# Kernel tuning notes

Measured on AMD Instinct MI355X. Metric: run time of the kernel, lower is better.

## Reference

```python
import jax, jax.numpy as jnp
import numpy as np

LEAKY_SLOPE = 0.01  # torch nn.LeakyReLU default


def leaky_relu(x):
    return jnp.where(x >= 0, x, LEAKY_SLOPE * x)


def rgcn_conv(x, edge_index, edge_type, w_rel, w_root, b_conv):
    # PyG RGCNConv: out = x @ W_root + b + sum_r mean_{edges of rel r into i}(x_src @ W_r)
    n = x.shape[0]
    src, dst = edge_index[0], edge_index[1]
    out = x @ w_root + b_conv
    num_rel = w_rel.shape[0]
    for r in range(num_rel):  # small fixed relation count
        mask = (edge_type == r)
        msg = x[src] @ w_rel[r]                      # [E, H]
        msg = jnp.where(mask[:, None], msg, 0.0)
        agg = jax.ops.segment_sum(msg, dst, num_segments=n)          # [N, H]
        cnt = jax.ops.segment_sum(mask.astype(x.dtype), dst, num_segments=n)
        out = out + agg / jnp.maximum(cnt, 1.0)[:, None]             # mean aggr
    return out


def setup_inputs() -> dict:
    key = jax.random.key(0)
    ks = jax.random.split(key, 10)
    N, E, D_IN, H, OUT, R = 50000, 600000, 768, 128, 3, 2
    s_in = 1.0 / np.sqrt(D_IN)
    s_h = 1.0 / np.sqrt(H)
    return {
        "feature": jax.random.normal(ks[0], (N, D_IN), dtype=jnp.float32),
        "edge_index": jax.random.randint(ks[1], (2, E), 0, N, dtype=jnp.int64),
        "edge_type": jax.random.randint(ks[2], (E,), 0, R, dtype=jnp.int64),
        "w_in": jax.random.uniform(ks[3], (D_IN, H), jnp.float32, -s_in, s_in),
        "b_in": jax.random.uniform(ks[4], (H,), jnp.float32, -s_in, s_in),
        "w_rel": jax.random.uniform(ks[5], (R, H, H), jnp.float32, -s_h, s_h),
        "w_root": jax.random.uniform(ks[6], (H, H), jnp.float32, -s_h, s_h),
        "b_conv": jnp.zeros((H,), jnp.float32),
        "w_out": jax.random.uniform(ks[7], (H, OUT), jnp.float32, -s_h, s_h),
        "b_out": jax.random.uniform(ks[8], (OUT,), jnp.float32, -s_h, s_h),
    }


def reference(feature, edge_index, edge_type, w_in, b_in, w_rel, w_root, b_conv, w_out, b_out):
    x = leaky_relu(feature @ w_in + b_in)
    # NOTE: original forward applies rgcn1 twice (shared weights); dropout is
    # identity at inference; rgcn2/linear_relu_output1 are unused.
    x = rgcn_conv(x, edge_index, edge_type, w_rel, w_root, b_conv)
    x = rgcn_conv(x, edge_index, edge_type, w_rel, w_root, b_conv)
    return x @ w_out + b_out
```

## Files before the change

### kernel.cpp

```cpp
#include <hip/hip_runtime.h>

#define H 128
#define CAP 64

typedef _Float16 f16x8 __attribute__((ext_vector_type(8)));
typedef float    f32x4 __attribute__((ext_vector_type(4)));

__global__ __launch_bounds__(256) void hist_fill(const int* __restrict__ src,
    const int* __restrict__ dst, const int* __restrict__ et,
    int* __restrict__ cnt, int* __restrict__ elist, int E, int N)
{
    int e = blockIdx.x * 256 + threadIdx.x;
    if (e >= E) return;
    int s = src[e], d = dst[e], t = et[e];
    int b = t * N + d;
    int pos = atomicAdd(&cnt[b], 1);
    if (pos < CAP) elist[(size_t)b * CAP + pos] = s;
}

__global__ __launch_bounds__(256) void prep_w(const float* __restrict__ w_in,
    const float* __restrict__ w_root, const float* __restrict__ w_rel,
    _Float16* __restrict__ wInT, _Float16* __restrict__ w3T, int K)
{
    int idx = blockIdx.x * 256 + threadIdx.x;
    int tot1 = K * H;
    if (idx < tot1) {
        int c = idx / K, k = idx - c * K;
        wInT[idx] = (_Float16)w_in[(size_t)k * H + c];
    } else {
        int i2 = idx - tot1;
        if (i2 < 3 * H * H) {
            int m = i2 / (H * H), r2 = i2 - m * (H * H);
            int c = r2 >> 7, k = r2 & 127;
            const float* s = (m == 0) ? w_root : (w_rel + (size_t)(m - 1) * H * H);
            w3T[i2] = (_Float16)s[(size_t)k * H + c];
        }
    }
}

__device__ __forceinline__ f16x8 cvt8(float4 v0, float4 v1) {
    f16x8 t;
    t[0] = (_Float16)v0.x; t[1] = (_Float16)v0.y; t[2] = (_Float16)v0.z; t[3] = (_Float16)v0.w;
    t[4] = (_Float16)v1.x; t[5] = (_Float16)v1.y; t[6] = (_Float16)v1.z; t[7] = (_Float16)v1.w;
    return t;
}

__global__ __launch_bounds__(256, 4) void gemm_big(const float* __restrict__ A,
    const _Float16* __restrict__ WT, const float* __restrict__ bias,
    _Float16* __restrict__ C16, int M, int K)
{
    __shared__ _Float16 As[2][64][40];
    __shared__ _Float16 Bs[2][128][40];

    const int tid = threadIdx.x;
    const int bm  = blockIdx.x * 64;
    const int w   = tid >> 6;
    const int l   = tid & 63;
    const int l15 = l & 15;
    const int q   = l >> 4;
    const int wr  = (w & 1) * 32;
    const int wc  = (w >> 1) * 64;

    const int sar = tid >> 2;
    const int sak = (tid & 3) * 8;
    int sarow = bm + sar; if (sarow >= M) sarow = M - 1;
    const float* ap = A + (size_t)sarow * K + sak;
    const int sbc = tid >> 1;
    const int sbk = (tid & 1) * 16;
    const _Float16* wp = WT + (size_t)sbc * K + sbk;

    f32x4 acc[2][4];
    const f32x4 z4 = {0.f, 0.f, 0.f, 0.f};
#pragma unroll
    for (int i = 0; i < 2; i++)
#pragma unroll
        for (int j = 0; j < 4; j++) acc[i][j] = z4;

    {
        float4 a0 = *(const float4*)(ap);
        float4 a1 = *(const float4*)(ap + 4);
        f16x8 b0  = *(const f16x8*)(wp);
        f16x8 b1  = *(const f16x8*)(wp + 8);
        *(f16x8*)&As[0][sar][sak]     = cvt8(a0, a1);
        *(f16x8*)&Bs[0][sbc][sbk]     = b0;
        *(f16x8*)&Bs[0][sbc][sbk + 8] = b1;
    }
    __syncthreads();

    const int steps = K / 32;
#pragma unroll 2
    for (int s = 0; s < steps; s++) {
        const int cur = s & 1;
        const bool more = (s + 1) < steps;
        float4 na0, na1; f16x8 nb0, nb1;
        if (more) {
            const int k0 = (s + 1) * 32;
            na0 = *(const float4*)(ap + k0);
            na1 = *(const float4*)(ap + k0 + 4);
            nb0 = *(const f16x8*)(wp + k0);
            nb1 = *(const f16x8*)(wp + k0 + 8);
        }
        f16x8 af[2], bf[4];
#pragma unroll
        for (int i = 0; i < 2; i++) af[i] = *(const f16x8*)&As[cur][wr + i * 16 + l15][q * 8];
#pragma unroll
        for (int j = 0; j < 4; j++) bf[j] = *(const f16x8*)&Bs[cur][wc + j * 16 + l15][q * 8];
#pragma unroll
        for (int i = 0; i < 2; i++)
#pragma unroll
            for (int j = 0; j < 4; j++)
                acc[i][j] = __builtin_amdgcn_mfma_f32_16x16x32_f16(af[i], bf[j], acc[i][j], 0, 0, 0);
        if (more) {
            *(f16x8*)&As[cur ^ 1][sar][sak]     = cvt8(na0, na1);
            *(f16x8*)&Bs[cur ^ 1][sbc][sbk]     = nb0;
            *(f16x8*)&Bs[cur ^ 1][sbc][sbk + 8] = nb1;
        }
        __syncthreads();
    }

#pragma unroll
    for (int j = 0; j < 4; j++) {
        int col = wc + j * 16 + l15;
        float bj = bias[col];
#pragma unroll
        for (int i = 0; i < 2; i++)
#pragma unroll
            for (int rg = 0; rg < 4; rg++) {
                int row = bm + wr + i * 16 + q * 4 + rg;
                if (row < M) {
                    float v = acc[i][j][rg] + bj;
                    v = (v >= 0.f) ? v : 0.01f * v;
                    C16[(size_t)row * H + col] = (_Float16)v;
                }
            }
    }
}

__global__ __launch_bounds__(512) void gemm3(const _Float16* __restrict__ X16,
    const _Float16* __restrict__ W3, const float* __restrict__ bias,
    float* __restrict__ Y, _Float16* __restrict__ Hh, int M, int mtiles,
    size_t NH)
{
    const int w   = threadIdx.x >> 6;
    const int l   = threadIdx.x & 63;
    const int l15 = l & 15;
    const int q   = l >> 4;
    const int col = w * 16 + l15;

    f16x8 bf[3][4];
#pragma unroll
    for (int m = 0; m < 3; m++) {
        const _Float16* wpp = W3 + (size_t)m * H * H + (size_t)col * H + q * 8;
#pragma unroll
        for (int c = 0; c < 4; c++) bf[m][c] = *(const f16x8*)(wpp + c * 32);
    }
    const float bj = bias[col];

    int t = blockIdx.x;
    if (t >= mtiles) return;
    f16x8 xf[4];
    {
        const _Float16* xp = X16 + ((size_t)t * 16 + l15) * H + q * 8;
#pragma unroll
        for (int c = 0; c < 4; c++) xf[c] = *(const f16x8*)(xp + c * 32);
    }

    const f32x4 z4 = {0.f, 0.f, 0.f, 0.f};
    while (true) {
        int tn = t + gridDim.x;
        bool more = tn < mtiles;
        f16x8 xnf[4];
        if (more) {
            const _Float16* xp = X16 + ((size_t)tn * 16 + l15) * H + q * 8;
#pragma unroll
            for (int c = 0; c < 4; c++) xnf[c] = *(const f16x8*)(xp + c * 32);
        }

        f32x4 a0 = z4, a1 = z4, a2 = z4;
#pragma unroll
        for (int c = 0; c < 4; c++) {
            a0 = __builtin_amdgcn_mfma_f32_16x16x32_f16(xf[c], bf[0][c], a0, 0, 0, 0);
            a1 = __builtin_amdgcn_mfma_f32_16x16x32_f16(xf[c], bf[1][c], a1, 0, 0, 0);
            a2 = __builtin_amdgcn_mfma_f32_16x16x32_f16(xf[c], bf[2][c], a2, 0, 0, 0);
        }

#pragma unroll
        for (int rg = 0; rg < 4; rg++) {
            int row = t * 16 + q * 4 + rg;
            if (row < M) {
                Y [(size_t)row * H + col]      = a0[rg] + bj;
                Hh[(size_t)row * H + col]      = (_Float16)a1[rg];
                Hh[NH + (size_t)row * H + col] = (_Float16)a2[rg];
            }
        }
        if (!more) break;
        t = tn;
#pragma unroll
        for (int c = 0; c < 4; c++) xf[c] = xnf[c];
    }
}

__global__ __launch_bounds__(256) void gather_mean(const float* __restrict__ Y,
    const _Float16* __restrict__ h, const int* __restrict__ elist,
    const int* __restrict__ cnt, _Float16* __restrict__ xn, int N, size_t NH)
{
    int wv = blockIdx.x * 4 + (threadIdx.x >> 6);
    int l  = threadIdx.x & 63;
    if (wv >= N) return;

    int d0r = cnt[wv], d1r = cnt[N + wv];
    int d0 = d0r < CAP ? d0r : CAP;
    int d1 = d1r < CAP ? d1r : CAP;
    float inv0 = d0r > 0 ? 1.f / (float)d0r : 0.f;
    float inv1 = d1r > 0 ? 1.f / (float)d1r : 0.f;
    const int* l0 = elist + (size_t)wv * CAP;
    const int* l1 = elist + ((size_t)N + wv) * CAP;
    const int tot = d0 + d1;

    const int eo = l >> 4;
    const int c8 = (l & 15) * 8;

    float acc[8];
#pragma unroll
    for (int j = 0; j < 8; j++) acc[j] = 0.f;

    for (int p = eo; p < tot; p += 8) {
        int pb = p + 4;
        bool fA = p < d0;
        int   sA  = fA ? l0[p] : l1[p - d0];
        float scA = fA ? inv0 : inv1;
        size_t hA = fA ? (size_t)0 : NH;
        f16x8 vA  = *(const f16x8*)&h[hA + (size_t)sA * H + c8];
        if (pb < tot) {
            bool fB = pb < d0;
            int   sB  = fB ? l0[pb] : l1[pb - d0];
            float scB = fB ? inv0 : inv1;
            size_t hB = fB ? (size_t)0 : NH;
            f16x8 vB  = *(const f16x8*)&h[hB + (size_t)sB * H + c8];
#pragma unroll
            for (int j = 0; j < 8; j++) acc[j] += scA * (float)vA[j] + scB * (float)vB[j];
        } else {
#pragma unroll
            for (int j = 0; j < 8; j++) acc[j] += scA * (float)vA[j];
        }
    }

#pragma unroll
    for (int j = 0; j < 8; j++) {
        acc[j] += __shfl_xor(acc[j], 16);
        acc[j] += __shfl_xor(acc[j], 32);
    }

    if (eo == 0) {
        float4 y0 = *(const float4*)&Y[(size_t)wv * H + c8];
        float4 y1 = *(const float4*)&Y[(size_t)wv * H + c8 + 4];
        f16x8 o;
        o[0] = (_Float16)(acc[0] + y0.x); o[1] = (_Float16)(acc[1] + y0.y);
        o[2] = (_Float16)(acc[2] + y0.z); o[3] = (_Float16)(acc[3] + y0.w);
        o[4] = (_Float16)(acc[4] + y1.x); o[5] = (_Float16)(acc[5] + y1.y);
        o[6] = (_Float16)(acc[6] + y1.z); o[7] = (_Float16)(acc[7] + y1.w);
        *(f16x8*)&xn[(size_t)wv * H + c8] = o;
    }
}

__global__ __launch_bounds__(256) void out_gemm(const _Float16* __restrict__ X16,
    const float* __restrict__ Wo, const float* __restrict__ bo,
    float* __restrict__ out, int N, int OUT)
{
    int row = blockIdx.x * 4 + (threadIdx.x >> 6);
    int lane = threadIdx.x & 63;
    if (row >= N) return;
    float a0 = (float)X16[(size_t)row * H + lane];
    float a1 = (float)X16[(size_t)row * H + 64 + lane];
    for (int c = 0; c < OUT; c++) {
        float p = a0 * Wo[lane * OUT + c] + a1 * Wo[(64 + lane) * OUT + c];
        for (int off = 32; off > 0; off >>= 1) p += __shfl_down(p, off);
        if (lane == 0) out[(size_t)row * OUT + c] = p + bo[c];
    }
}

extern "C" void kernel_launch(void* const* d_in, const int* in_sizes, int n_in,
                              void* d_out, int out_size, void* d_ws, size_t ws_size,
                              hipStream_t stream) {
    const float* feature = (const float*)d_in[0];
    const int*   ei      = (const int*)d_in[1];
    const int*   et      = (const int*)d_in[2];
    const float* w_in    = (const float*)d_in[3];
    const float* b_in    = (const float*)d_in[4];
    const float* w_rel   = (const float*)d_in[5];
    const float* w_root  = (const float*)d_in[6];
    const float* b_conv  = (const float*)d_in[7];
    const float* w_out   = (const float*)d_in[8];
    const float* b_out   = (const float*)d_in[9];

    const int HH   = in_sizes[4];
    const int D_IN = in_sizes[3] / HH;
    const int N    = in_sizes[0] / D_IN;
    const int E    = in_sizes[1] / 2;
    const int R    = in_sizes[5] / (HH * HH);
    const int OUT  = in_sizes[9];

    const size_t NH = (size_t)N * H;

    char* base = (char*)d_ws;
    _Float16* wInT = (_Float16*)base;
    _Float16* w3T  = wInT + (size_t)D_IN * HH;
    _Float16* x0   = w3T + (size_t)3 * HH * HH;
    _Float16* x1   = x0 + NH;
    _Float16* h    = x1 + NH;
    float* y       = (float*)(h + (size_t)R * NH);
    int* cnt       = (int*)(y + NH);
    int* elist     = cnt + (size_t)R * N;

    hipMemsetAsync(cnt, 0, sizeof(int) * (size_t)R * N, stream);
    prep_w<<<(D_IN * HH + 3 * HH * HH + 255) / 256, 256, 0, stream>>>(
        w_in, w_root, w_rel, wInT, w3T, D_IN);
    hist_fill<<<(E + 255) / 256, 256, 0, stream>>>(ei, ei + E, et, cnt, elist, E, N);

    gemm_big<<<(N + 63) / 64, 256, 0, stream>>>(feature, wInT, b_in, x0, N, D_IN);

    const int mtiles = (N + 15) / 16;
    _Float16* xc = x0;
    _Float16* xo = x1;
    for (int layer = 0; layer < 2; layer++) {
        gemm3<<<1024, 512, 0, stream>>>(xc, w3T, b_conv, y, h, N, mtiles, NH);
        gather_mean<<<(N + 3) / 4, 256, 0, stream>>>(y, h, elist, cnt, xo, N, NH);
        _Float16* t = xc; xc = xo; xo = t;
    }

    out_gemm<<<(N + 3) / 4, 256, 0, stream>>>(xc, w_out, b_out, (float*)d_out, N, OUT);
}
```

Measured before the change: 465.4 us.

## Drop LDS staging in input GEMM; load MFMA fragments directly from pre-packed weights

Repacks W_in in the prep kernel into an MFMA-fragment-friendly layout so each lane can load its B fragments with contiguous 16-byte reads. The input GEMM now loads A rows and B fragments straight from global memory into registers, with no shared memory and no per-step barriers. Each wave computes a 32x128 tile, so each block covers 128 rows. This removes LDS traffic and synchronization, but each wave now reads the full weight tile from global/L2 on its own, and register pressure goes up (launch bound lowered to 2).

```diff
diff --git a/kernel.cpp b/kernel.cpp
--- a/kernel.cpp
+++ b/kernel.cpp
@@ -25,8 +25,9 @@
     int idx = blockIdx.x * 256 + threadIdx.x;
     int tot1 = K * H;
     if (idx < tot1) {
-        int c = idx / K, k = idx - c * K;
-        wInT[idx] = (_Float16)w_in[(size_t)k * H + c];
+        int k = idx >> 7, c = idx & 127;
+        int o = ((k >> 3) << 10) + (c << 3) + (k & 7);
+        wInT[o] = (_Float16)w_in[idx];
     } else {
         int i2 = idx - tot1;
         if (i2 < 3 * H * H) {
@@ -45,95 +46,85 @@
     return t;
 }
 
-__global__ __launch_bounds__(256, 4) void gemm_big(const float* __restrict__ A,
-    const _Float16* __restrict__ WT, const float* __restrict__ bias,
+__global__ __launch_bounds__(256, 2) void gemm_big(const float* __restrict__ A,
+    const _Float16* __restrict__ WP, const float* __restrict__ bias,
     _Float16* __restrict__ C16, int M, int K)
 {
-    __shared__ _Float16 As[2][64][40];
-    __shared__ _Float16 Bs[2][128][40];
-
     const int tid = threadIdx.x;
-    const int bm  = blockIdx.x * 64;
     const int w   = tid >> 6;
     const int l   = tid & 63;
     const int l15 = l & 15;
     const int q   = l >> 4;
-    const int wr  = (w & 1) * 32;
-    const int wc  = (w >> 1) * 64;
-
-    const int sar = tid >> 2;
-    const int sak = (tid & 3) * 8;
-    int sarow = bm + sar; if (sarow >= M) sarow = M - 1;
-    const float* ap = A + (size_t)sarow * K + sak;
-    const int sbc = tid >> 1;
-    const int sbk = (tid & 1) * 16;
-    const _Float16* wp = WT + (size_t)sbc * K + sbk;
-
-    f32x4 acc[2][4];
+    const int brow = blockIdx.x * 128 + w * 32;
+
+    int r0 = brow + l15;      if (r0 >= M) r0 = M - 1;
+    int r1 = brow + 16 + l15; if (r1 >= M) r1 = M - 1;
+    const float* ap0 = A + (size_t)r0 * K + q * 8;
+    const float* ap1 = A + (size_t)r1 * K + q * 8;
+    const _Float16* bp = WP + ((size_t)q * H + l15) * 8;
+
+    float bj[8];
+#pragma unroll
+    for (int j = 0; j < 8; j++) bj[j] = bias[j * 16 + l15];
+
+    f32x4 acc[2][8];
     const f32x4 z4 = {0.f, 0.f, 0.f, 0.f};
 #pragma unroll
     for (int i = 0; i < 2; i++)
 #pragma unroll
-        for (int j = 0; j < 4; j++) acc[i][j] = z4;
-
-    {
-        float4 a0 = *(const float4*)(ap);
-        float4 a1 = *(const float4*)(ap + 4);
-        f16x8 b0  = *(const f16x8*)(wp);
-        f16x8 b1  = *(const f16x8*)(wp + 8);
-        *(f16x8*)&As[0][sar][sak]     = cvt8(a0, a1);
-        *(f16x8*)&Bs[0][sbc][sbk]     = b0;
-        *(f16x8*)&Bs[0][sbc][sbk + 8] = b1;
-    }
-    __syncthreads();
+        for (int j = 0; j < 8; j++) acc[i][j] = z4;
+
+    float4 a00 = *(const float4*)(ap0);
+    float4 a01 = *(const float4*)(ap0 + 4);
+    float4 a10 = *(const float4*)(ap1);
+    float4 a11 = *(const float4*)(ap1 + 4);
+    f16x8 bf[8];
+#pragma unroll
+    for (int j = 0; j < 8; j++) bf[j] = *(const f16x8*)(bp + j * 128);
 
     const int steps = K / 32;
 #pragma unroll 2
     for (int s = 0; s < steps; s++) {
-        const int cur = s & 1;
         const bool more = (s + 1) < steps;
-        float4 na0, na1; f16x8 nb0, nb1;
+        float4 na00, na01, na10, na11; f16x8 nbf[8];
         if (more) {
             const int k0 = (s + 1) * 32;
-            na0 = *(const float4*)(ap + k0);
-            na1 = *(const float4*)(ap + k0 + 4);
-            nb0 = *(const f16x8*)(wp + k0);
-            nb1 = *(const f16x8*)(wp + k0 + 8);
-        }
-        f16x8 af[2], bf[4];
-#pragma unroll
-        for (int i = 0; i < 2; i++) af[i] = *(const f16x8*)&As[cur][wr + i * 16 + l15][q * 8];
-#pragma unroll
-        for (int j = 0; j < 4; j++) bf[j] = *(const f16x8*)&Bs[cur][wc + j * 16 + l15][q * 8];
-#pragma unroll
-        for (int i = 0; i < 2; i++)
-#pragma unroll
-            for (int j = 0; j < 4; j++)
-                acc[i][j] = __builtin_amdgcn_mfma_f32_16x16x32_f16(af[i], bf[j], acc[i][j], 0, 0, 0);
+            na00 = *(const float4*)(ap0 + k0);
+            na01 = *(const float4*)(ap0 + k0 + 4);
+            na10 = *(const float4*)(ap1 + k0);
+            na11 = *(const float4*)(ap1 + k0 + 4);
+            const _Float16* nb = bp + (size_t)(s + 1) * 4 * H * 8;
+#pragma unroll
+            for (int j = 0; j < 8; j++) nbf[j] = *(const f16x8*)(nb + j * 128);
+        }
+        f16x8 af0 = cvt8(a00, a01);
+        f16x8 af1 = cvt8(a10, a11);
+#pragma unroll
+        for (int j = 0; j < 8; j++) {
+            acc[0][j] = __builtin_amdgcn_mfma_f32_16x16x32_f16(af0, bf[j], acc[0][j], 0, 0, 0);
+            acc[1][j] = __builtin_amdgcn_mfma_f32_16x16x32_f16(af1, bf[j], acc[1][j], 0, 0, 0);
+        }
         if (more) {
-            *(f16x8*)&As[cur ^ 1][sar][sak]     = cvt8(na0, na1);
-            *(f16x8*)&Bs[cur ^ 1][sbc][sbk]     = nb0;
-            *(f16x8*)&Bs[cur ^ 1][sbc][sbk + 8] = nb1;
-        }
-        __syncthreads();
-    }
-
-#pragma unroll
-    for (int j = 0; j < 4; j++) {
-        int col = wc + j * 16 + l15;
-        float bj = bias[col];
-#pragma unroll
-        for (int i = 0; i < 2; i++)
-#pragma unroll
-            for (int rg = 0; rg < 4; rg++) {
-                int row = bm + wr + i * 16 + q * 4 + rg;
-                if (row < M) {
-                    float v = acc[i][j][rg] + bj;
+            a00 = na00; a01 = na01; a10 = na10; a11 = na11;
+#pragma unroll
+            for (int j = 0; j < 8; j++) bf[j] = nbf[j];
+        }
+    }
+
+#pragma unroll
+    for (int i = 0; i < 2; i++)
+#pragma unroll
+        for (int rg = 0; rg < 4; rg++) {
+            int row = brow + i * 16 + q * 4 + rg;
+            if (row < M) {
+#pragma unroll
+                for (int j = 0; j < 8; j++) {
+                    float v = acc[i][j][rg] + bj[j];
                     v = (v >= 0.f) ? v : 0.01f * v;
-                    C16[(size_t)row * H + col] = (_Float16)v;
+                    C16[(size_t)row * H + j * 16 + l15] = (_Float16)v;
                 }
             }
-    }
+        }
 }
 
 __global__ __launch_bounds__(512) void gemm3(const _Float16* __restrict__ X16,
@@ -317,7 +308,7 @@
         w_in, w_root, w_rel, wInT, w3T, D_IN);
     hist_fill<<<(E + 255) / 256, 256, 0, stream>>>(ei, ei + E, et, cnt, elist, E, N);
 
-    gemm_big<<<(N + 63) / 64, 256, 0, stream>>>(feature, wInT, b_in, x0, N, D_IN);
+    gemm_big<<<(N + 127) / 128, 256, 0, stream>>>(feature, wInT, b_in, x0, N, D_IN);
 
     const int mtiles = (N + 15) / 16;
     _Float16* xc = x0;
```

Result: faster. 456.3 us (-2.0%).
